# Kernel tuning notes

Hardware: AMD Instinct MI355X
Metric: run time of the kernel (lower is better)

Reference implementation:

```python
import jax, jax.numpy as jnp
import numpy as np

NUM_NODES = 50000
NUM_EDGES = 800000
NUM_LABEL_EDGES = 100000
F_IN, F_HID, F_OUT = 128, 128, 64


def gcn_conv(x, src, dst, W, b, n):
    # PyG GCNConv: h = x @ W; add self-loops; symmetric normalization
    # deg counted on destination (col), including self-loop (+1).
    h = x @ W
    deg = jax.ops.segment_sum(jnp.ones(src.shape, h.dtype), dst, num_segments=n) + 1.0
    dinv = jax.lax.rsqrt(deg)  # deg >= 1 always (self-loop)
    norm = dinv[src] * dinv[dst]                       # [E]
    agg = jax.ops.segment_sum(h[src] * norm[:, None], dst, num_segments=n)
    agg = agg + h * (dinv * dinv)[:, None]             # self-loop term dinv[i]^2 * h[i]
    return agg + b


def setup_inputs() -> dict:
    key = jax.random.key(0)
    ks = jax.random.split(key, 9)
    x = jax.random.normal(ks[0], (NUM_NODES, F_IN), dtype=jnp.float32)
    edge_index = jax.random.randint(ks[1], (2, NUM_EDGES), 0, NUM_NODES, dtype=jnp.int64)
    edge_label_index = jax.random.randint(ks[2], (2, NUM_LABEL_EDGES), 0, NUM_NODES, dtype=jnp.int64)
    def glorot(k, fi, fo):
        s = (6.0 / (fi + fo)) ** 0.5
        return jax.random.uniform(k, (fi, fo), jnp.float32, -s, s)
    return {
        "x": x,
        "edge_index": edge_index,
        "edge_label_index": edge_label_index,
        "W1": glorot(ks[3], F_IN, F_HID),  "b1": jnp.zeros((F_HID,), jnp.float32),
        "W2": glorot(ks[4], F_HID, F_HID), "b2": jnp.zeros((F_HID,), jnp.float32),
        "W3": glorot(ks[5], F_HID, F_OUT), "b3": jnp.zeros((F_OUT,), jnp.float32),
    }


def reference(x, edge_index, edge_label_index, W1, b1, W2, b2, W3, b3):
    src, dst = edge_index[0], edge_index[1]
    z = jax.nn.relu(gcn_conv(x, src, dst, W1, b1, NUM_NODES))
    z = jax.nn.relu(gcn_conv(z, src, dst, W2, b2, NUM_NODES))
    z = gcn_conv(z, src, dst, W3, b3, NUM_NODES)
    # decode: dot product of endpoint embeddings per label edge
    return jnp.sum(z[edge_label_index[0]] * z[edge_label_index[1]], axis=-1)
```

## Files before the change

kernel.cpp:

```cpp
#include <hip/hip_runtime.h>
#include <hip/hip_bf16.h>
#include <stdint.h>

#define NN 50000
#define NE 800000
#define NL 100000
#define SLOTS 64
#define PADROW 50000

#define NB 196
#define BSH 8
#define BCAP 5376

typedef __attribute__((ext_vector_type(8))) short bf16x8;
typedef __attribute__((ext_vector_type(4))) float f32x4;
typedef __attribute__((ext_vector_type(4))) unsigned int u32x4;
typedef __attribute__((ext_vector_type(2))) unsigned int u32x2;
typedef __attribute__((ext_vector_type(8))) unsigned short u16x8;

__device__ __forceinline__ float asf(unsigned int u) {
    union { unsigned int i; float f; } c; c.i = u; return c.f;
}
__device__ __forceinline__ float bflo(unsigned int x) { return asf(x << 16); }
__device__ __forceinline__ float bfhi(unsigned int x) { return asf(x & 0xffff0000u); }
__device__ __forceinline__ unsigned short f2bf(float f) {
    union { float f; unsigned int i; } c; c.f = f;
    unsigned int u = c.i + (0x7fffu + ((c.i >> 16) & 1u));
    return (unsigned short)(u >> 16);
}

__device__ __forceinline__ void dma16(const unsigned short* g, char* l) {
    __builtin_amdgcn_global_load_lds(
        (const __attribute__((address_space(1))) unsigned int*)g,
        (__attribute__((address_space(3))) unsigned int*)l, 16, 0, 0);
}

__global__ void k_wprep(const float* __restrict__ W1, const float* __restrict__ W2,
                        const float* __restrict__ W3, unsigned short* __restrict__ Wt,
                        int* __restrict__ cursor, unsigned int* __restrict__ padA,
                        unsigned int* __restrict__ padB) {
    int idx = blockIdx.x * 256 + threadIdx.x;
    if (idx < NB) cursor[idx] = 0;
    if (idx < 64) padA[idx] = 0;
    else if (idx < 128) padB[idx - 64] = 0;
    const float* W; unsigned short* O; int base, Mloc;
    if (idx < 16384)      { W = W1; O = Wt;         base = idx;         Mloc = 128; }
    else if (idx < 32768) { W = W2; O = Wt + 16384; base = idx - 16384; Mloc = 128; }
    else                  { W = W3; O = Wt + 32768; base = idx - 32768; Mloc = 64;  }
    int n = base >> 7, k = base & 127;
    O[base] = f2bf(W[k * Mloc + n]);
}

__global__ __launch_bounds__(256) void k_bin(
        const int* __restrict__ src, const int* __restrict__ dst,
        int* __restrict__ cursor, unsigned int* __restrict__ binbuf) {
    __shared__ int hcnt[NB];
    __shared__ int hbase[NB];
    __shared__ unsigned int epk[2048];
    int tid = threadIdx.x;
    if (tid < NB) hcnt[tid] = 0;
    __syncthreads();
    int e0 = blockIdx.x * 2048;
    int e1 = min(e0 + 2048, NE);
    for (int e = e0 + tid; e < e1; e += 256) {
        int d = dst[e], s = src[e];
        atomicAdd(&hcnt[d >> BSH], 1);
        epk[e - e0] = (unsigned int)s | ((unsigned int)d << 16);
    }
    __syncthreads();
    if (tid < NB) { hbase[tid] = atomicAdd(&cursor[tid], hcnt[tid]); hcnt[tid] = 0; }
    __syncthreads();
    for (int e = e0 + tid; e < e1; e += 256) {
        unsigned int pk = epk[e - e0];
        int b = (int)(pk >> 16) >> BSH;
        int p = hbase[b] + atomicAdd(&hcnt[b], 1);
        if (p < BCAP)
            __builtin_nontemporal_store(pk, &binbuf[(size_t)b * BCAP + p]);
    }
}

__global__ __launch_bounds__(256) void k_csr(
        const unsigned int* __restrict__ binbuf, const int* __restrict__ cursor,
        int* __restrict__ deg, unsigned short* __restrict__ colp) {
    __shared__ unsigned short lcol[256 * SLOTS];
    __shared__ int ldeg[256];
    int tid = threadIdx.x;
    int blk = blockIdx.x;
    int base = blk << BSH;
    int nNodes = min(256, NN - base);
    ldeg[tid] = 0;
    const unsigned int fw = 0xC350C350u;
    u32x4 fill = {fw, fw, fw, fw};
    u32x4* lz = (u32x4*)lcol;
#pragma unroll
    for (int i = 0; i < 8; ++i) lz[i * 256 + tid] = fill;
    __syncthreads();
    int cnt = min(cursor[blk], BCAP);
    for (int e = tid; e < cnt; e += 256) {
        unsigned int pk = __builtin_nontemporal_load(&binbuf[(size_t)blk * BCAP + e]);
        int d = (int)(pk >> 16) - base;
        int p = atomicAdd(&ldeg[d], 1);
        if (p < SLOTS) {
            int pp = (p < 32) ? ((p & 3) * 8 + (p >> 2)) : p;
            lcol[d * SLOTS + pp] = (unsigned short)(pk & 0xffffu);
        }
    }
    __syncthreads();
    if (tid < nNodes) {
        int dv = ldeg[tid];
        deg[base + tid] = dv;
        if (dv < SLOTS) {
            int pp = (dv < 32) ? ((dv & 3) * 8 + (dv >> 2)) : dv;
            lcol[tid * SLOTS + pp] = (unsigned short)(base + tid);
        }
    }
    __syncthreads();
    u32x4* gout = (u32x4*)(colp + (size_t)base * SLOTS);
    const u32x4* lin = (const u32x4*)lcol;
    for (int i = tid; i < nNodes * 8; i += 256) gout[i] = lin[i];
}

__global__ __launch_bounds__(256) void k_gemm1(
        const float* __restrict__ A, const unsigned short* __restrict__ Wt,
        const int* __restrict__ deg, unsigned short* __restrict__ Outb, int N) {
    constexpr int K = 128;
    constexpr int NT = 8;
    int tid = threadIdx.x;
    int lane = tid & 63, wave = tid >> 6;
    int m = lane & 15, quad = lane >> 4;
    int rowA = blockIdx.x * 64 + wave * 16 + m;
    int rA = min(rowA, N - 1);

    bf16x8 afr[4];
    const float* p = A + (size_t)rA * K + quad * 8;
#pragma unroll
    for (int s = 0; s < 4; ++s) {
        float4 lo = *(const float4*)(p + s * 32);
        float4 hi = *(const float4*)(p + s * 32 + 4);
        bf16x8 r;
        r[0] = (short)f2bf(lo.x); r[1] = (short)f2bf(lo.y);
        r[2] = (short)f2bf(lo.z); r[3] = (short)f2bf(lo.w);
        r[4] = (short)f2bf(hi.x); r[5] = (short)f2bf(hi.y);
        r[6] = (short)f2bf(hi.z); r[7] = (short)f2bf(hi.w);
        afr[s] = r;
    }

    f32x4 acc[NT];
#pragma unroll
    for (int t = 0; t < NT; ++t) { acc[t][0] = 0.f; acc[t][1] = 0.f; acc[t][2] = 0.f; acc[t][3] = 0.f; }
#pragma unroll
    for (int t = 0; t < NT; ++t) {
        const unsigned short* wp = Wt + (size_t)(t * 16 + m) * K + quad * 8;
#pragma unroll
        for (int s = 0; s < 4; ++s) {
            bf16x8 bfr = *(const bf16x8*)(wp + s * 32);
            acc[t] = __builtin_amdgcn_mfma_f32_16x16x32_bf16(afr[s], bfr, acc[t], 0, 0, 0);
        }
    }

    int outRowBase = blockIdx.x * 64 + wave * 16 + quad * 4;
    float di[4];
#pragma unroll
    for (int i = 0; i < 4; ++i) di[i] = rsqrtf((float)deg[min(outRowBase + i, N - 1)] + 1.0f);
#pragma unroll
    for (int t = 0; t < NT; ++t)
#pragma unroll
        for (int i = 0; i < 4; ++i) {
            int rr = outRowBase + i;
            if (rr < N) Outb[(size_t)rr * 128 + t * 16 + m] = f2bf(acc[t][i] * di[i]);
        }
}

template <int M_>
__global__ __launch_bounds__(256, 4) void k_agg_gemm(
        const unsigned short* __restrict__ hs, const int* __restrict__ deg,
        const unsigned short* __restrict__ colp, const float* __restrict__ bias,
        const unsigned short* __restrict__ Wt, unsigned short* __restrict__ Outb) {
    constexpr int K = 128;
    constexpr int NT = M_ / 64;
    __shared__ __align__(16) unsigned short As[16][136];
    __shared__ __align__(16) char stage[4][8192];
    int tid = threadIdx.x;
    int lane = tid & 63, wave = tid >> 6;
    int tileBase = blockIdx.x * 16;
    int g = lane >> 4, c = lane & 15;
    const unsigned short* hc = hs + c * 8;
    int nodeB = tileBase + wave * 4;

    int4 dg = *(const int4*)(deg + nodeB);
    int dgv[4] = {dg.x, dg.y, dg.z, dg.w};
    u16x8 sl4[4];
#pragma unroll
    for (int t = 0; t < 4; ++t)
        sl4[t] = *(const u16x8*)(colp + (unsigned)(nodeB + t) * SLOTS + g * 8);

    char* sb = &stage[wave][0];

#pragma unroll
    for (int t = 0; t < 4; ++t) {
        int node = nodeB + t;
        int su = min(dgv[t] + 1, SLOTS);

#pragma unroll
        for (int j = 0; j < 8; ++j)
            if (4 * j < su)
                dma16(hc + (unsigned)sl4[t][j] * K, sb + j * 1024);

        float acc[8];
#pragma unroll
        for (int k = 0; k < 8; ++k) acc[k] = 0.f;

        if (su > 32) {
            u16x8 s2 = *(const u16x8*)(colp + (unsigned)node * SLOTS + 32 + g * 8);
#pragma unroll
            for (int h = 0; h < 8; ++h) {
                u32x4 x = *(const u32x4*)(hc + (unsigned)s2[h] * K);
#pragma unroll
                for (int k = 0; k < 4; ++k) {
                    acc[2 * k]     += bflo(x[k]);
                    acc[2 * k + 1] += bfhi(x[k]);
                }
            }
        }

        asm volatile("s_waitcnt vmcnt(0)" ::: "memory");

#pragma unroll
        for (int j = 0; j < 8; ++j) {
            if (4 * j < su) {
                u32x4 v = *(const u32x4*)(sb + j * 1024 + g * 256 + c * 16);
#pragma unroll
                for (int k = 0; k < 4; ++k) {
                    acc[2 * k]     += bflo(v[k]);
                    acc[2 * k + 1] += bfhi(v[k]);
                }
            }
        }

#pragma unroll
        for (int k = 0; k < 8; ++k) {
            acc[k] += __shfl_xor(acc[k], 16, 64);
            acc[k] += __shfl_xor(acc[k], 32, 64);
        }
        if (g == 0) {
            float di = rsqrtf((float)dgv[t] + 1.0f);
            const float4* bp = (const float4*)(bias + c * 8);
            float4 b0 = bp[0], b1 = bp[1];
            float bb[8] = {b0.x, b0.y, b0.z, b0.w, b1.x, b1.y, b1.z, b1.w};
            u32x4 pv;
#pragma unroll
            for (int k = 0; k < 4; ++k) {
                float o0 = fmaxf(di * acc[2 * k]     + bb[2 * k],     0.f);
                float o1 = fmaxf(di * acc[2 * k + 1] + bb[2 * k + 1], 0.f);
                pv[k] = (unsigned int)f2bf(o0) | ((unsigned int)f2bf(o1) << 16);
            }
            *(u32x4*)&As[wave * 4 + t][c * 8] = pv;
        }
    }
    __syncthreads();

    int m = lane & 15, quad = lane >> 4;
    bf16x8 afr[4];
#pragma unroll
    for (int s = 0; s < 4; ++s)
        afr[s] = *(const bf16x8*)&As[m][s * 32 + quad * 8];

    f32x4 gacc[NT];
#pragma unroll
    for (int t = 0; t < NT; ++t) { gacc[t][0] = 0.f; gacc[t][1] = 0.f; gacc[t][2] = 0.f; gacc[t][3] = 0.f; }
#pragma unroll
    for (int t = 0; t < NT; ++t) {
        int ct = wave * NT + t;
        const unsigned short* wp = Wt + (size_t)(ct * 16 + m) * K + quad * 8;
#pragma unroll
        for (int s = 0; s < 4; ++s) {
            bf16x8 bfr = *(const bf16x8*)(wp + s * 32);
            gacc[t] = __builtin_amdgcn_mfma_f32_16x16x32_bf16(afr[s], bfr, gacc[t], 0, 0, 0);
        }
    }

    int rowBase = tileBase + quad * 4;
    int4 dg2 = *(const int4*)(deg + rowBase);
    int dgw[4] = {dg2.x, dg2.y, dg2.z, dg2.w};
    float di[4];
#pragma unroll
    for (int i = 0; i < 4; ++i) di[i] = rsqrtf((float)dgw[i] + 1.0f);
#pragma unroll
    for (int t = 0; t < NT; ++t) {
        int ct = wave * NT + t;
#pragma unroll
        for (int i = 0; i < 4; ++i)
            Outb[(size_t)(rowBase + i) * M_ + ct * 16 + m] = f2bf(gacc[t][i] * di[i]);
    }
}

__global__ __launch_bounds__(256, 8) void k_agg64(
        const unsigned short* __restrict__ hs, const int* __restrict__ deg,
        const unsigned short* __restrict__ colp, const float* __restrict__ bias,
        unsigned short* __restrict__ out, int n) {
    int tid = threadIdx.x;
    int wave = tid >> 6, lane = tid & 63;
    int node = blockIdx.x * 4 + wave;
    int g = lane >> 4, c = lane & 15;
    const unsigned short* hc = hs + c * 4;

    int degv = deg[node];
    int su = min(degv + 1, SLOTS);
    u16x8 sl = *(const u16x8*)(colp + (unsigned)node * SLOTS + g * 8);

    u32x2 vv[6];
#pragma unroll
    for (int k2 = 0; k2 < 6; ++k2)
        vv[k2] = *(const u32x2*)(hc + (unsigned)sl[k2] * 64);

    float acc[4] = {0.f, 0.f, 0.f, 0.f};
#pragma unroll
    for (int k2 = 0; k2 < 6; ++k2)
#pragma unroll
        for (int k = 0; k < 2; ++k) {
            acc[2 * k]     += bflo(vv[k2][k]);
            acc[2 * k + 1] += bfhi(vv[k2][k]);
        }
    if (su > 24) {
        u32x2 w0 = *(const u32x2*)(hc + (unsigned)sl[6] * 64);
        u32x2 w1 = *(const u32x2*)(hc + (unsigned)sl[7] * 64);
#pragma unroll
        for (int k = 0; k < 2; ++k) {
            acc[2 * k]     += bflo(w0[k]) + bflo(w1[k]);
            acc[2 * k + 1] += bfhi(w0[k]) + bfhi(w1[k]);
        }
        if (su > 32) {
            u16x8 s2 = *(const u16x8*)(colp + (unsigned)node * SLOTS + 32 + g * 8);
#pragma unroll
            for (int h = 0; h < 2; ++h) {
                u32x2 x0 = *(const u32x2*)(hc + (unsigned)s2[4 * h + 0] * 64);
                u32x2 x1 = *(const u32x2*)(hc + (unsigned)s2[4 * h + 1] * 64);
                u32x2 x2 = *(const u32x2*)(hc + (unsigned)s2[4 * h + 2] * 64);
                u32x2 x3 = *(const u32x2*)(hc + (unsigned)s2[4 * h + 3] * 64);
#pragma unroll
                for (int k = 0; k < 2; ++k) {
                    acc[2 * k]     += bflo(x0[k]) + bflo(x1[k]) + bflo(x2[k]) + bflo(x3[k]);
                    acc[2 * k + 1] += bfhi(x0[k]) + bfhi(x1[k]) + bfhi(x2[k]) + bfhi(x3[k]);
                }
            }
        }
    }
#pragma unroll
    for (int k = 0; k < 4; ++k) {
        acc[k] += __shfl_xor(acc[k], 16, 64);
        acc[k] += __shfl_xor(acc[k], 32, 64);
    }
    if (g == 0) {
        float di = rsqrtf((float)degv + 1.0f);
        float4 bb = *(const float4*)(bias + c * 4);
        u32x2 pv;
        pv[0] = (unsigned int)f2bf(di * acc[0] + bb.x) |
                ((unsigned int)f2bf(di * acc[1] + bb.y) << 16);
        pv[1] = (unsigned int)f2bf(di * acc[2] + bb.z) |
                ((unsigned int)f2bf(di * acc[3] + bb.w) << 16);
        *(u32x2*)(out + (size_t)node * 64 + c * 4) = pv;
    }
}

__global__ __launch_bounds__(256) void k_decode(
        const unsigned short* __restrict__ z, const int* __restrict__ ls,
        const int* __restrict__ ld, float* __restrict__ out, int nl) {
    int tid = threadIdx.x;
    int lane = tid & 63, wave = tid >> 6;
    int g = lane >> 3, c = lane & 7;
    int e = (blockIdx.x * 4 + wave) * 4 + (g >> 1);
    int row = (g & 1) ? ld[e] : ls[e];
    u32x4 v = *(const u32x4*)(z + (size_t)row * 64 + c * 8);
    u32x4 w;
#pragma unroll
    for (int k = 0; k < 4; ++k) w[k] = (unsigned int)__shfl_xor((int)v[k], 8, 64);
    float p = 0.f;
#pragma unroll
    for (int k = 0; k < 4; ++k)
        p += bflo(v[k]) * bflo(w[k]) + bfhi(v[k]) * bfhi(w[k]);
    p += __shfl_xor(p, 1, 64);
    p += __shfl_xor(p, 2, 64);
    p += __shfl_xor(p, 4, 64);
    if ((lane & 15) == 0) out[e] = p;
}


static inline size_t align256(size_t x) { return (x + 255) & ~(size_t)255; }

extern "C" void kernel_launch(void* const* d_in, const int* in_sizes, int n_in,
                              void* d_out, int out_size, void* d_ws, size_t ws_size,
                              hipStream_t stream) {
    const float* x  = (const float*)d_in[0];
    const int*   ei = (const int*)d_in[1];
    const int*   li = (const int*)d_in[2];
    const float* W1 = (const float*)d_in[3];
    const float* b1 = (const float*)d_in[4];
    const float* W2 = (const float*)d_in[5];
    const float* b2 = (const float*)d_in[6];
    const float* W3 = (const float*)d_in[7];
    const float* b3 = (const float*)d_in[8];
    float* out = (float*)d_out;

    const int* src = ei;
    const int* dst = ei + NE;
    const int* ls = li;
    const int* ld = li + NL;

    char* ws = (char*)d_ws;
    size_t off = 0;
    int* deg    = (int*)(ws + off); off += align256(NN * 4);
    int* cursor = (int*)(ws + off); off += align256(NB * 4);
    unsigned int* binbuf = (unsigned int*)(ws + off); off += align256((size_t)NB * BCAP * 4);
    unsigned short* colp = (unsigned short*)(ws + off); off += align256((size_t)NN * SLOTS * 2);
    unsigned short* Wtb  = (unsigned short*)(ws + off); off += align256(40960 * 2);
    unsigned short* bufA = (unsigned short*)(ws + off); off += align256(((size_t)NN * 128 + 128) * 2);
    unsigned short* bufB = (unsigned short*)(ws + off); off += align256(((size_t)NN * 128 + 128) * 2);
    unsigned short* bufZ = (unsigned short*)(ws + off); off += align256((size_t)NN * 64 * 2);
    unsigned short* h3 = bufA + (size_t)25000 * 128;

    k_wprep<<<160, 256, 0, stream>>>(W1, W2, W3, Wtb, cursor,
                                     (unsigned int*)(bufA + (size_t)PADROW * 128),
                                     (unsigned int*)(bufB + (size_t)PADROW * 128));
    k_bin<<<391, 256, 0, stream>>>(src, dst, cursor, binbuf);
    k_csr<<<NB, 256, 0, stream>>>(binbuf, cursor, deg, colp);

    k_gemm1<<<782, 256, 0, stream>>>(x, Wtb, deg, bufA, NN);
    k_agg_gemm<128><<<3125, 256, 0, stream>>>(bufA, deg, colp, b1, Wtb + 16384, bufB);
    k_agg_gemm<64><<<3125, 256, 0, stream>>>(bufB, deg, colp, b2, Wtb + 32768, h3);
    k_agg64<<<12500, 256, 0, stream>>>(h3, deg, colp, b3, bufZ, NN);
    k_decode<<<6250, 256, 0, stream>>>(bufZ, ls, ld, out, NL);
}
```

Before: 247.8 us.

## Double-buffer neighbor-row DMA staging across nodes in aggregation-GEMM kernel

Restructures the per-wave gather in k_agg_gemm so the first 6 slot groups of the next node are prefetched into a second LDS buffer while the current node is accumulated. Slot groups 6-7 are now read directly from global memory, and the waits use partial vmcnt counts instead of draining everything. The bias load is hoisted out of the node loop and the occupancy hint is dropped from launch_bounds. This aims to hide gather latency behind accumulation, at the cost of unconditional DMAs for low-degree nodes, fragile vmcnt bookkeeping, and possibly higher register use.

```diff
diff --git a/kernel.cpp b/kernel.cpp
--- a/kernel.cpp
+++ b/kernel.cpp
@@ -172,14 +172,14 @@
 }
 
 template <int M_>
-__global__ __launch_bounds__(256, 4) void k_agg_gemm(
+__global__ __launch_bounds__(256) void k_agg_gemm(
         const unsigned short* __restrict__ hs, const int* __restrict__ deg,
         const unsigned short* __restrict__ colp, const float* __restrict__ bias,
         const unsigned short* __restrict__ Wt, unsigned short* __restrict__ Outb) {
     constexpr int K = 128;
     constexpr int NT = M_ / 64;
     __shared__ __align__(16) unsigned short As[16][136];
-    __shared__ __align__(16) char stage[4][8192];
+    __shared__ __align__(16) char stage[4][2][6144];
     int tid = threadIdx.x;
     int lane = tid & 63, wave = tid >> 6;
     int tileBase = blockIdx.x * 16;
@@ -194,47 +194,72 @@
     for (int t = 0; t < 4; ++t)
         sl4[t] = *(const u16x8*)(colp + (unsigned)(nodeB + t) * SLOTS + g * 8);
 
-    char* sb = &stage[wave][0];
+    float bb[8];
+    {
+        const float4* bp = (const float4*)(bias + c * 8);
+        float4 b0 = bp[0], b1 = bp[1];
+        bb[0] = b0.x; bb[1] = b0.y; bb[2] = b0.z; bb[3] = b0.w;
+        bb[4] = b1.x; bb[5] = b1.y; bb[6] = b1.z; bb[7] = b1.w;
+    }
+
+#pragma unroll
+    for (int j = 0; j < 6; ++j)
+        dma16(hc + (unsigned)sl4[0][j] * K, &stage[wave][0][j * 1024]);
+#pragma unroll
+    for (int j = 0; j < 6; ++j)
+        dma16(hc + (unsigned)sl4[1][j] * K, &stage[wave][1][j * 1024]);
 
 #pragma unroll
     for (int t = 0; t < 4; ++t) {
         int node = nodeB + t;
         int su = min(dgv[t] + 1, SLOTS);
 
-#pragma unroll
-        for (int j = 0; j < 8; ++j)
-            if (4 * j < su)
-                dma16(hc + (unsigned)sl4[t][j] * K, sb + j * 1024);
-
+        if (t < 3) asm volatile("s_waitcnt vmcnt(6)" ::: "memory");
+        else       asm volatile("s_waitcnt vmcnt(0)" ::: "memory");
+        __builtin_amdgcn_sched_barrier(0);
+
+        const char* sb = &stage[wave][t & 1][0];
         float acc[8];
 #pragma unroll
         for (int k = 0; k < 8; ++k) acc[k] = 0.f;
-
-        if (su > 32) {
-            u16x8 s2 = *(const u16x8*)(colp + (unsigned)node * SLOTS + 32 + g * 8);
-#pragma unroll
-            for (int h = 0; h < 8; ++h) {
-                u32x4 x = *(const u32x4*)(hc + (unsigned)s2[h] * K);
-#pragma unroll
-                for (int k = 0; k < 4; ++k) {
-                    acc[2 * k]     += bflo(x[k]);
-                    acc[2 * k + 1] += bfhi(x[k]);
+#pragma unroll
+        for (int j = 0; j < 6; ++j) {
+            u32x4 v = *(const u32x4*)(sb + j * 1024 + g * 256 + c * 16);
+#pragma unroll
+            for (int k = 0; k < 4; ++k) {
+                acc[2 * k]     += bflo(v[k]);
+                acc[2 * k + 1] += bfhi(v[k]);
+            }
+        }
+
+        if (su > 24) {
+            u32x4 w0 = *(const u32x4*)(hc + (unsigned)sl4[t][6] * K);
+            u32x4 w1 = *(const u32x4*)(hc + (unsigned)sl4[t][7] * K);
+#pragma unroll
+            for (int k = 0; k < 4; ++k) {
+                acc[2 * k]     += bflo(w0[k]) + bflo(w1[k]);
+                acc[2 * k + 1] += bfhi(w0[k]) + bfhi(w1[k]);
+            }
+            if (su > 32) {
+                u16x8 s2 = *(const u16x8*)(colp + (unsigned)node * SLOTS + 32 + g * 8);
+#pragma unroll
+                for (int h = 0; h < 8; ++h) {
+                    u32x4 x = *(const u32x4*)(hc + (unsigned)s2[h] * K);
+#pragma unroll
+                    for (int k = 0; k < 4; ++k) {
+                        acc[2 * k]     += bflo(x[k]);
+                        acc[2 * k + 1] += bfhi(x[k]);
+                    }
                 }
             }
         }
 
-        asm volatile("s_waitcnt vmcnt(0)" ::: "memory");
-
-#pragma unroll
-        for (int j = 0; j < 8; ++j) {
-            if (4 * j < su) {
-                u32x4 v = *(const u32x4*)(sb + j * 1024 + g * 256 + c * 16);
-#pragma unroll
-                for (int k = 0; k < 4; ++k) {
-                    acc[2 * k]     += bflo(v[k]);
-                    acc[2 * k + 1] += bfhi(v[k]);
-                }
-            }
+        __builtin_amdgcn_sched_barrier(0);
+        if (t < 2) {
+#pragma unroll
+            for (int j = 0; j < 6; ++j)
+                dma16(hc + (unsigned)sl4[t + 2][j] * K,
+                      &stage[wave][t & 1][j * 1024]);
         }
 
 #pragma unroll
@@ -244,9 +269,6 @@
         }
         if (g == 0) {
             float di = rsqrtf((float)dgv[t] + 1.0f);
-            const float4* bp = (const float4*)(bias + c * 8);
-            float4 b0 = bp[0], b1 = bp[1];
-            float bb[8] = {b0.x, b0.y, b0.z, b0.w, b1.x, b1.y, b1.z, b1.w};
             u32x4 pv;
 #pragma unroll
             for (int k = 0; k < 4; ++k) {
```

After: 237.0 us. 4.4% less time.
